# Kernel optimization log

Measured on AMD Instinct MI355X. Metric: run time of the kernel, lower is better.

## Reference

```python
import jax, jax.numpy as jnp
import numpy as np

B, S, H, O = 128, 1000, 256, 2


def setup_inputs() -> dict:
    key = jax.random.key(0)
    ks = jax.random.split(key, 14)
    scale = 0.05
    return {
        "decoder_input": jax.random.normal(ks[0], (B, O), jnp.float32),
        "last_hidden": jax.random.normal(ks[1], (B, H), jnp.float32),
        "static": jax.random.normal(ks[2], (B, S, H), jnp.float32),
        "dynamic": jax.random.normal(ks[3], (B, S, H), jnp.float32),
        "emb_W": jax.random.normal(ks[4], (H, O), jnp.float32) * scale,
        "emb_b": jnp.zeros((H,), jnp.float32),
        "gru_Wih": jax.random.normal(ks[5], (3 * H, H), jnp.float32) * scale,
        "gru_Whh": jax.random.normal(ks[6], (3 * H, H), jnp.float32) * scale,
        "gru_bih": jnp.zeros((3 * H,), jnp.float32),
        "gru_bhh": jnp.zeros((3 * H,), jnp.float32),
        "attn_W": jax.random.normal(ks[7], (3 * H, 3 * H), jnp.float32) * scale,
        "attn_v": jax.random.normal(ks[8], (3 * H,), jnp.float32) * scale,
        "dec_W": jax.random.normal(ks[9], (2 * H, 2 * H), jnp.float32) * scale,
        "dec_v": jax.random.normal(ks[10], (2 * H,), jnp.float32) * scale,
    }


def _gru_cell(x, h, Wih, Whh, bih, bhh):
    # PyTorch GRU gate order: r, z, n
    gx = x @ Wih.T + bih          # [B, 3H]
    gh = h @ Whh.T + bhh          # [B, 3H]
    xr, xz, xn = jnp.split(gx, 3, axis=-1)
    hr, hz, hn = jnp.split(gh, 3, axis=-1)
    r = jax.nn.sigmoid(xr + hr)
    z = jax.nn.sigmoid(xz + hz)
    n = jnp.tanh(xn + r * hn)
    return (1.0 - z) * n + z * h


def reference(decoder_input, last_hidden, static, dynamic,
              emb_W, emb_b, gru_Wih, gru_Whh, gru_bih, gru_bhh,
              attn_W, attn_v, dec_W, dec_v):
    # Embed decoder input and run one GRU step
    embedded = decoder_input @ emb_W.T + emb_b                      # [B, H]
    h_new = _gru_cell(embedded, last_hidden, gru_Wih, gru_Whh, gru_bih, gru_bhh)  # [B, H]

    # Attention: v . tanh(W @ concat(static, dynamic, hidden)) per (b, s)
    hid = jnp.broadcast_to(h_new[:, None, :], static.shape)         # [B, S, H]
    cat = jnp.concatenate([static, dynamic, hid], axis=-1)          # [B, S, 3H]
    scores = jnp.tanh(jnp.einsum('bsk,jk->bsj', cat, attn_W)) @ attn_v  # [B, S]
    attn = jax.nn.softmax(scores, axis=1)

    # Context: attention-weighted sum of static encodings
    context = jnp.einsum('bs,bsh->bh', attn, static)                # [B, H]

    # Final pointer scorer over concat(static, context)
    ctx = jnp.broadcast_to(context[:, None, :], static.shape)
    cat2 = jnp.concatenate([static, ctx], axis=-1)                  # [B, S, 2H]
    out_scores = jnp.tanh(jnp.einsum('bsk,jk->bsj', cat2, dec_W)) @ dec_v  # [B, S]
    outputs = jax.nn.softmax(out_scores, axis=1)
    hidden = h_new[None]                                            # [1, B, H]
    return outputs, hidden
```

## Files before the change

kernel.cpp:

```cpp
#include <hip/hip_runtime.h>

#define BB 128
#define SS 1000
#define HH 256
#define H3 768
#define H2 512
#define NCHUNK 8

typedef unsigned short u16;
typedef short short8 __attribute__((ext_vector_type(8)));
typedef float floatx4 __attribute__((ext_vector_type(4)));
typedef u16 ushort4v __attribute__((ext_vector_type(4)));

__device__ __forceinline__ float bf2f(u16 u) {
    union { unsigned int i; float f; } v;
    v.i = ((unsigned int)u) << 16;
    return v.f;
}

__device__ __forceinline__ u16 f2bf(float f) {
    unsigned int x = __float_as_uint(f);
    x += 0x7FFFu + ((x >> 16) & 1u);
    return (u16)(x >> 16);
}

__device__ __forceinline__ float fast_tanh(float x) {
    float t = __expf(2.0f * x);
    return 1.0f - 2.0f * __builtin_amdgcn_rcpf(t + 1.0f);
}

__device__ __forceinline__ float sigmoidf(float x) {
    return __builtin_amdgcn_rcpf(1.0f + __expf(-x));
}

__device__ __forceinline__ void gl2lds16(const void* src, void* dst) {
    __builtin_amdgcn_global_load_lds(
        (const __attribute__((address_space(1))) unsigned int*)src,
        (__attribute__((address_space(3))) unsigned int*)dst,
        16, 0, 0);
}

__global__ __launch_bounds__(256) void k_prep(
    const float* __restrict__ aW, const float* __restrict__ dW,
    u16* __restrict__ aWb, u16* __restrict__ dWb)
{
    int idx = (blockIdx.x * 256 + threadIdx.x) * 4;
    const float* src;
    u16* dst;
    if (idx < 589824) { src = aW + idx; dst = aWb + idx; }
    else              { src = dW + (idx - 589824); dst = dWb + (idx - 589824); }
    float4 v = *(const float4*)src;
    ushort4v o = { f2bf(v.x), f2bf(v.y), f2bf(v.z), f2bf(v.w) };
    *(ushort4v*)dst = o;
}

__global__ __launch_bounds__(256) void k_gru(
    const float* __restrict__ dec, const float* __restrict__ h0,
    const float* __restrict__ embW, const float* __restrict__ embb,
    const float* __restrict__ Wih, const float* __restrict__ Whh,
    const float* __restrict__ bih, const float* __restrict__ bhh,
    const float* __restrict__ attnW,
    float* __restrict__ Wh, float* __restrict__ out_hidden)
{
    const int b = blockIdx.x, t = threadIdx.x;
    __shared__ float emb_s[HH], h_s[HH], hn_s[HH];

    const float d0 = dec[b * 2 + 0], d1 = dec[b * 2 + 1];
    emb_s[t] = d0 * embW[t * 2 + 0] + d1 * embW[t * 2 + 1] + embb[t];
    h_s[t] = h0[b * HH + t];
    __syncthreads();

    auto dotrow = [&](const float* Wr, const float* xs) -> float {
        float acc = 0.f;
        const float4* p = (const float4*)Wr;
#pragma unroll 8
        for (int c = 0; c < HH / 4; ++c) {
            float4 w = p[c];
            acc += w.x * xs[c * 4 + 0] + w.y * xs[c * 4 + 1]
                 + w.z * xs[c * 4 + 2] + w.w * xs[c * 4 + 3];
        }
        return acc;
    };

    float gr = dotrow(Wih + (size_t)t * HH, emb_s) + bih[t]
             + dotrow(Whh + (size_t)t * HH, h_s) + bhh[t];
    float r = sigmoidf(gr);

    float gz = dotrow(Wih + (size_t)(HH + t) * HH, emb_s) + bih[HH + t]
             + dotrow(Whh + (size_t)(HH + t) * HH, h_s) + bhh[HH + t];
    float z = sigmoidf(gz);

    float xn = dotrow(Wih + (size_t)(2 * HH + t) * HH, emb_s) + bih[2 * HH + t];
    float hn = dotrow(Whh + (size_t)(2 * HH + t) * HH, h_s) + bhh[2 * HH + t];
    float n = fast_tanh(xn + r * hn);

    float hv = (1.0f - z) * n + z * h_s[t];
    out_hidden[b * HH + t] = hv;
    hn_s[t] = hv;
    __syncthreads();

#pragma unroll
    for (int rr = 0; rr < 3; ++rr) {
        int j = t + rr * HH;
        Wh[b * H3 + j] = dotrow(attnW + (size_t)j * H3 + 2 * HH, hn_s);
    }
}

template <int KSTEPS, int NTILES, int WSTRIDE>
__global__ __launch_bounds__(256, 2) void k_scores(
    const float* __restrict__ A1, const float* __restrict__ A2,
    const u16* __restrict__ Wb, const float* __restrict__ addj,
    const float* __restrict__ vj, float* __restrict__ out)
{
    constexpr int GPR    = KSTEPS * 4;
    constexpr int NINSTR = KSTEPS / 2;
    constexpr int BUFU16 = 1024 * KSTEPS;
    constexpr int NG     = NTILES / 2;
    constexpr int NJ     = NTILES * 16;

    __shared__ u16 smem[2 * BUFU16];
    __shared__ float aj_s[NJ], vj_s[NJ];

    const int b = blockIdx.y, t = threadIdx.x;
    const int wave = t >> 6, lane = t & 63;
    const int q = lane >> 4, c = lane & 15;
    const int swz = c & 7;
    const int s_base = blockIdx.x * 128 + wave * 32;
    const int kb = q * 8;

    auto stage = [&](int g, int bufsel) {
        const int jbase = g * 32;
        u16* base = smem + bufsel * BUFU16;
#pragma unroll
        for (int i = 0; i < NINSTR; ++i) {
            int gl = (wave * NINSTR + i) * 64 + lane;
            int r  = gl / GPR;
            int p  = gl % GPR;
            int gg = p ^ (r & 7);
            const u16* src = Wb + (size_t)(jbase + r) * WSTRIDE + gg * 8;
            u16* dst = base + (size_t)(wave * NINSTR + i) * 512;
            gl2lds16(src, dst);
        }
    };
    stage(0, 0);

    for (int i = t; i < NJ; i += 256) {
        aj_s[i] = addj[b * NJ + i];
        vj_s[i] = vj[i];
    }

    short8 afrag[2][KSTEPS];
#pragma unroll
    for (int mt = 0; mt < 2; ++mt) {
        int row = s_base + mt * 16 + c;
        if (row > SS - 1) row = SS - 1;
        const size_t abase = (size_t)(b * SS + row) * HH;
#pragma unroll
        for (int ks = 0; ks < KSTEPS; ++ks) {
            int k = ks * 32 + kb;
            const float* src = (k < HH) ? (A1 + abase + k) : (A2 + abase + (k - HH));
            float4 u0 = *(const float4*)src;
            float4 u1 = *(const float4*)(src + 4);
            short8 f;
            f[0] = (short)f2bf(u0.x); f[1] = (short)f2bf(u0.y);
            f[2] = (short)f2bf(u0.z); f[3] = (short)f2bf(u0.w);
            f[4] = (short)f2bf(u1.x); f[5] = (short)f2bf(u1.y);
            f[6] = (short)f2bf(u1.z); f[7] = (short)f2bf(u1.w);
            afrag[mt][ks] = f;
        }
    }

    float pout[2][4] = {{0.f, 0.f, 0.f, 0.f}, {0.f, 0.f, 0.f, 0.f}};
    floatx4 accB[2][2][2];

    auto epilogue = [&](int gg) {
        floatx4 (*ac)[2] = accB[gg & 1];
#pragma unroll
        for (int jt = 0; jt < 2; ++jt) {
            const int j = gg * 32 + jt * 16 + c;
            const float aj = aj_s[j];
            const float vv = vj_s[j];
#pragma unroll
            for (int r4 = 0; r4 < 4; ++r4) {
                pout[0][r4] += fast_tanh(ac[jt][0][r4] + aj) * vv;
                pout[1][r4] += fast_tanh(ac[jt][1][r4] + aj) * vv;
            }
        }
    };

    int have = 0, gP = 0;
    for (int g = 0; g < NG; ++g) {
        __syncthreads();
        if (g + 1 < NG) stage(g + 1, (g + 1) & 1);

        const u16* base = smem + (g & 1) * BUFU16;
        floatx4 (*acc)[2] = accB[g & 1];
#pragma unroll
        for (int jt = 0; jt < 2; ++jt)
#pragma unroll
            for (int mt = 0; mt < 2; ++mt)
                acc[jt][mt] = (floatx4){0.f, 0.f, 0.f, 0.f};

        auto ldsrd = [&](int ks, int jt) -> short8 {
            const int paddr = ((jt * 16 + c) * GPR + ((ks * 4 + q) ^ swz)) * 8;
            return *(const short8*)(base + paddr);
        };

        short8 wf0 = ldsrd(0, 0);
        short8 wf1 = ldsrd(0, 1);

        if (have) epilogue(gP);

#pragma unroll
        for (int ks = 0; ks < KSTEPS; ++ks) {
            short8 nf0, nf1;
            if (ks + 1 < KSTEPS) { nf0 = ldsrd(ks + 1, 0); nf1 = ldsrd(ks + 1, 1); }
            acc[0][0] = __builtin_amdgcn_mfma_f32_16x16x32_bf16(afrag[0][ks], wf0, acc[0][0], 0, 0, 0);
            acc[0][1] = __builtin_amdgcn_mfma_f32_16x16x32_bf16(afrag[1][ks], wf0, acc[0][1], 0, 0, 0);
            acc[1][0] = __builtin_amdgcn_mfma_f32_16x16x32_bf16(afrag[0][ks], wf1, acc[1][0], 0, 0, 0);
            acc[1][1] = __builtin_amdgcn_mfma_f32_16x16x32_bf16(afrag[1][ks], wf1, acc[1][1], 0, 0, 0);
            wf0 = nf0; wf1 = nf1;
        }
        gP = g; have = 1;
    }
    epilogue(gP);

#pragma unroll
    for (int mt = 0; mt < 2; ++mt)
#pragma unroll
        for (int r4 = 0; r4 < 4; ++r4)
#pragma unroll
            for (int off = 1; off < 16; off <<= 1)
                pout[mt][r4] += __shfl_xor(pout[mt][r4], off, 64);

    if (c == 0) {
#pragma unroll
        for (int mt = 0; mt < 2; ++mt) {
            const int srow = s_base + mt * 16 + q * 4;
#pragma unroll
            for (int r4 = 0; r4 < 4; ++r4)
                if (srow + r4 < SS) out[b * SS + srow + r4] = pout[mt][r4];
        }
    }
}

__global__ __launch_bounds__(256) void k_softmax(
    const float* __restrict__ in, float* __restrict__ outf)
{
    const int b = blockIdx.x, t = threadIdx.x;
    __shared__ float red[4];
    const float* rowp = in + b * SS;

    float m = -1e30f;
    for (int s = t; s < SS; s += 256) m = fmaxf(m, rowp[s]);
#pragma unroll
    for (int off = 32; off >= 1; off >>= 1) m = fmaxf(m, __shfl_xor(m, off, 64));
    if ((t & 63) == 0) red[t >> 6] = m;
    __syncthreads();
    m = fmaxf(fmaxf(red[0], red[1]), fmaxf(red[2], red[3]));

    float sum = 0.f;
    for (int s = t; s < SS; s += 256) sum += __expf(rowp[s] - m);
#pragma unroll
    for (int off = 32; off >= 1; off >>= 1) sum += __shfl_xor(sum, off, 64);
    __syncthreads();
    if ((t & 63) == 0) red[t >> 6] = sum;
    __syncthreads();
    sum = red[0] + red[1] + red[2] + red[3];

    const float inv = 1.0f / sum;
    for (int s = t; s < SS; s += 256)
        outf[b * SS + s] = __expf(rowp[s] - m) * inv;
}

__global__ __launch_bounds__(256) void k_ctx_part(
    const float* __restrict__ attn, const float* __restrict__ stat,
    float* __restrict__ part)
{
    constexpr int CH = SS / NCHUNK;
    const int chunk = blockIdx.x, b = blockIdx.y, t = threadIdx.x;
    const int wave = t >> 6, lane = t & 63;

    __shared__ float attn_s[CH];
    __shared__ float red[4][HH];

    for (int i = t; i < CH; i += 256) attn_s[i] = attn[b * SS + chunk * CH + i];
    __syncthreads();

    float4 acc = {0.f, 0.f, 0.f, 0.f};
    const float* base = stat + ((size_t)(b * SS + chunk * CH) * HH) + lane * 4;
#pragma unroll 4
    for (int i = wave; i < CH; i += 4) {
        float w = attn_s[i];
        float4 v = *(const float4*)(base + (size_t)i * HH);
        acc.x += w * v.x; acc.y += w * v.y; acc.z += w * v.z; acc.w += w * v.w;
    }
    *(float4*)(&red[wave][lane * 4]) = acc;
    __syncthreads();

    part[(size_t)(chunk * BB + b) * HH + t] =
        red[0][t] + red[1][t] + red[2][t] + red[3][t];
}

__global__ __launch_bounds__(256) void k_ctx_red(
    const float* __restrict__ part, const u16* __restrict__ decWb,
    float* __restrict__ Dc)
{
    const int b = blockIdx.x, t = threadIdx.x;
    __shared__ float ctx_s[HH];

    float s = 0.f;
#pragma unroll
    for (int c = 0; c < NCHUNK; ++c) s += part[(size_t)(c * BB + b) * HH + t];
    ctx_s[t] = s;
    __syncthreads();

#pragma unroll
    for (int rr = 0; rr < 2; ++rr) {
        int j = t + rr * 256;
        float a2 = 0.f;
        const short8* p = (const short8*)(decWb + (size_t)j * H2 + HH);
#pragma unroll 4
        for (int cc = 0; cc < HH / 8; ++cc) {
            short8 w = p[cc];
#pragma unroll
            for (int k = 0; k < 8; ++k) a2 += bf2f((u16)w[k]) * ctx_s[cc * 8 + k];
        }
        Dc[b * H2 + j] = a2;
    }
}

extern "C" void kernel_launch(void* const* d_in, const int* in_sizes, int n_in,
                              void* d_out, int out_size, void* d_ws, size_t ws_size,
                              hipStream_t stream)
{
    const float* dec   = (const float*)d_in[0];
    const float* h0    = (const float*)d_in[1];
    const float* stat  = (const float*)d_in[2];
    const float* dyn   = (const float*)d_in[3];
    const float* embW  = (const float*)d_in[4];
    const float* embb  = (const float*)d_in[5];
    const float* Wih   = (const float*)d_in[6];
    const float* Whh   = (const float*)d_in[7];
    const float* bih   = (const float*)d_in[8];
    const float* bhh   = (const float*)d_in[9];
    const float* attnW = (const float*)d_in[10];
    const float* attnv = (const float*)d_in[11];
    const float* decW  = (const float*)d_in[12];
    const float* decv  = (const float*)d_in[13];

    float* out        = (float*)d_out;
    float* out_probs  = out;
    float* out_hidden = out + BB * SS;

    u16* wsb     = (u16*)d_ws;
    u16* attnWb  = wsb;
    u16* decWb   = wsb + 589824;
    float* wsf   = (float*)(wsb + 851968);
    float* Wh      = wsf;
    float* scores  = wsf + 98304;
    float* attn    = wsf + 226304;
    float* Dc      = wsf + 354304;
    float* oscores = wsf + 419840;
    float* ctxpart = wsf + 547840;

    k_prep<<<832, 256, 0, stream>>>(attnW, decW, attnWb, decWb);
    k_gru<<<BB, 256, 0, stream>>>(dec, h0, embW, embb, Wih, Whh, bih, bhh,
                                  attnW, Wh, out_hidden);
    k_scores<16, 48, H3><<<dim3(8, BB), 256, 0, stream>>>(stat, dyn, attnWb, Wh,
                                                          attnv, scores);
    k_softmax<<<BB, 256, 0, stream>>>(scores, attn);
    k_ctx_part<<<dim3(NCHUNK, BB), 256, 0, stream>>>(attn, stat, ctxpart);
    k_ctx_red<<<BB, 256, 0, stream>>>(ctxpart, decWb, Dc);
    k_scores<8, 32, H2><<<dim3(8, BB), 256, 0, stream>>>(stat, nullptr, decWb, Dc,
                                                         decv, oscores);
    k_softmax<<<BB, 256, 0, stream>>>(oscores, out_probs);
}
```

Before: 609.4 us.

## Shrink k_scores j-tile to 16 columns and raise occupancy bounds

The scoring kernel now processes one 16-column weight tile per pipeline stage instead of two. It drops the deferred double-buffered accumulators and applies the tanh epilogue right after each tile's MFMAs. This cuts the accumulator register footprint and halves the LDS buffer, allowing launch bounds of 3 and 4 waves per EU, and the second call's loads lose the A1/A2 select at compile time. In exchange there are twice as many barriers and stage iterations. The epilogue also no longer overlaps the next tile's MFMAs, so latency hiding depends on the higher occupancy.

```diff
diff --git a/kernel.cpp b/kernel.cpp
--- a/kernel.cpp
+++ b/kernel.cpp
@@ -106,17 +106,17 @@
     }
 }
 
-template <int KSTEPS, int NTILES, int WSTRIDE>
-__global__ __launch_bounds__(256, 2) void k_scores(
+template <int KSTEPS, int NT16, int WSTRIDE, int MINW>
+__global__ __launch_bounds__(256, MINW) void k_scores(
     const float* __restrict__ A1, const float* __restrict__ A2,
     const u16* __restrict__ Wb, const float* __restrict__ addj,
     const float* __restrict__ vj, float* __restrict__ out)
 {
     constexpr int GPR    = KSTEPS * 4;
-    constexpr int NINSTR = KSTEPS / 2;
-    constexpr int BUFU16 = 1024 * KSTEPS;
-    constexpr int NG     = NTILES / 2;
-    constexpr int NJ     = NTILES * 16;
+    constexpr int NINSTR = KSTEPS / 4;
+    constexpr int BUFU16 = 512 * KSTEPS;
+    constexpr int NG     = NT16;
+    constexpr int NJ     = NT16 * 16;
 
     __shared__ u16 smem[2 * BUFU16];
     __shared__ float aj_s[NJ], vj_s[NJ];
@@ -129,7 +129,7 @@
     const int kb = q * 8;
 
     auto stage = [&](int g, int bufsel) {
-        const int jbase = g * 32;
+        const int jbase = g * 16;
         u16* base = smem + bufsel * BUFU16;
 #pragma unroll
         for (int i = 0; i < NINSTR; ++i) {
@@ -138,7 +138,7 @@
             int p  = gl % GPR;
             int gg = p ^ (r & 7);
             const u16* src = Wb + (size_t)(jbase + r) * WSTRIDE + gg * 8;
-            u16* dst = base + (size_t)(wave * NINSTR + i) * 512;
+            u16* dst = base + (wave * NINSTR + i) * 512;
             gl2lds16(src, dst);
         }
     };
@@ -158,7 +158,12 @@
 #pragma unroll
         for (int ks = 0; ks < KSTEPS; ++ks) {
             int k = ks * 32 + kb;
-            const float* src = (k < HH) ? (A1 + abase + k) : (A2 + abase + (k - HH));
+            const float* src;
+            if constexpr (KSTEPS * 32 <= HH) {
+                src = A1 + abase + k;
+            } else {
+                src = (k < HH) ? (A1 + abase + k) : (A2 + abase + (k - HH));
+            }
             float4 u0 = *(const float4*)src;
             float4 u1 = *(const float4*)(src + 4);
             short8 f;
@@ -171,59 +176,39 @@
     }
 
     float pout[2][4] = {{0.f, 0.f, 0.f, 0.f}, {0.f, 0.f, 0.f, 0.f}};
-    floatx4 accB[2][2][2];
-
-    auto epilogue = [&](int gg) {
-        floatx4 (*ac)[2] = accB[gg & 1];
-#pragma unroll
-        for (int jt = 0; jt < 2; ++jt) {
-            const int j = gg * 32 + jt * 16 + c;
-            const float aj = aj_s[j];
-            const float vv = vj_s[j];
-#pragma unroll
-            for (int r4 = 0; r4 < 4; ++r4) {
-                pout[0][r4] += fast_tanh(ac[jt][0][r4] + aj) * vv;
-                pout[1][r4] += fast_tanh(ac[jt][1][r4] + aj) * vv;
-            }
-        }
-    };
-
-    int have = 0, gP = 0;
+
     for (int g = 0; g < NG; ++g) {
         __syncthreads();
         if (g + 1 < NG) stage(g + 1, (g + 1) & 1);
 
         const u16* base = smem + (g & 1) * BUFU16;
-        floatx4 (*acc)[2] = accB[g & 1];
-#pragma unroll
-        for (int jt = 0; jt < 2; ++jt)
-#pragma unroll
-            for (int mt = 0; mt < 2; ++mt)
-                acc[jt][mt] = (floatx4){0.f, 0.f, 0.f, 0.f};
-
-        auto ldsrd = [&](int ks, int jt) -> short8 {
-            const int paddr = ((jt * 16 + c) * GPR + ((ks * 4 + q) ^ swz)) * 8;
+        floatx4 acc0 = {0.f, 0.f, 0.f, 0.f};
+        floatx4 acc1 = {0.f, 0.f, 0.f, 0.f};
+
+        auto ldsrd = [&](int ks) -> short8 {
+            const int paddr = (c * GPR + ((ks * 4 + q) ^ swz)) * 8;
             return *(const short8*)(base + paddr);
         };
 
-        short8 wf0 = ldsrd(0, 0);
-        short8 wf1 = ldsrd(0, 1);
-
-        if (have) epilogue(gP);
-
+        short8 wf = ldsrd(0);
 #pragma unroll
         for (int ks = 0; ks < KSTEPS; ++ks) {
-            short8 nf0, nf1;
-            if (ks + 1 < KSTEPS) { nf0 = ldsrd(ks + 1, 0); nf1 = ldsrd(ks + 1, 1); }
-            acc[0][0] = __builtin_amdgcn_mfma_f32_16x16x32_bf16(afrag[0][ks], wf0, acc[0][0], 0, 0, 0);
-            acc[0][1] = __builtin_amdgcn_mfma_f32_16x16x32_bf16(afrag[1][ks], wf0, acc[0][1], 0, 0, 0);
-            acc[1][0] = __builtin_amdgcn_mfma_f32_16x16x32_bf16(afrag[0][ks], wf1, acc[1][0], 0, 0, 0);
-            acc[1][1] = __builtin_amdgcn_mfma_f32_16x16x32_bf16(afrag[1][ks], wf1, acc[1][1], 0, 0, 0);
-            wf0 = nf0; wf1 = nf1;
-        }
-        gP = g; have = 1;
-    }
-    epilogue(gP);
+            short8 nf;
+            if (ks + 1 < KSTEPS) nf = ldsrd(ks + 1);
+            acc0 = __builtin_amdgcn_mfma_f32_16x16x32_bf16(afrag[0][ks], wf, acc0, 0, 0, 0);
+            acc1 = __builtin_amdgcn_mfma_f32_16x16x32_bf16(afrag[1][ks], wf, acc1, 0, 0, 0);
+            wf = nf;
+        }
+
+        const int j = g * 16 + c;
+        const float aj = aj_s[j];
+        const float vv = vj_s[j];
+#pragma unroll
+        for (int r4 = 0; r4 < 4; ++r4) {
+            pout[0][r4] += fast_tanh(acc0[r4] + aj) * vv;
+            pout[1][r4] += fast_tanh(acc1[r4] + aj) * vv;
+        }
+    }
 
 #pragma unroll
     for (int mt = 0; mt < 2; ++mt)
@@ -367,12 +352,12 @@
     k_prep<<<832, 256, 0, stream>>>(attnW, decW, attnWb, decWb);
     k_gru<<<BB, 256, 0, stream>>>(dec, h0, embW, embb, Wih, Whh, bih, bhh,
                                   attnW, Wh, out_hidden);
-    k_scores<16, 48, H3><<<dim3(8, BB), 256, 0, stream>>>(stat, dyn, attnWb, Wh,
-                                                          attnv, scores);
+    k_scores<16, 48, H3, 3><<<dim3(8, BB), 256, 0, stream>>>(stat, dyn, attnWb, Wh,
+                                                             attnv, scores);
     k_softmax<<<BB, 256, 0, stream>>>(scores, attn);
     k_ctx_part<<<dim3(NCHUNK, BB), 256, 0, stream>>>(attn, stat, ctxpart);
     k_ctx_red<<<BB, 256, 0, stream>>>(ctxpart, decWb, Dc);
-    k_scores<8, 32, H2><<<dim3(8, BB), 256, 0, stream>>>(stat, nullptr, decWb, Dc,
-                                                         decv, oscores);
+    k_scores<8, 32, H2, 4><<<dim3(8, BB), 256, 0, stream>>>(stat, nullptr, decWb, Dc,
+                                                            decv, oscores);
     k_softmax<<<BB, 256, 0, stream>>>(oscores, out_probs);
 }
```

After: 705.0 us. +15.7%, slower.
